# Kernel tuning notes

Measured on AMD Instinct MI355X. Metric: run time of the kernel, lower is better.

Reference implementation:

```python
import jax, jax.numpy as jnp
import numpy as np

N_NODES = 100000
N_EDGES = 1600000
IN_FEATS = 128
N_HIDDEN = 64
N_HEADS = 4
N_CLASSES = 16


def setup_inputs() -> dict:
    key = jax.random.key(0)
    ks = jax.random.split(key, 16)
    h = jax.random.normal(ks[0], (N_NODES, IN_FEATS), dtype=jnp.float32)
    src = jax.random.randint(ks[1], (N_EDGES,), 0, N_NODES, dtype=jnp.int32)
    dst = jax.random.randint(ks[2], (N_EDGES,), 0, N_NODES, dtype=jnp.int32)
    def xavier(k, shape, fan_in, fan_out):
        gain = jnp.sqrt(2.0)  # calculate_gain('relu')
        std = gain * jnp.sqrt(2.0 / (fan_in + fan_out))
        return (std * jax.random.normal(k, shape)).astype(jnp.float32)
    # layer 1: per-head W [H, in, out], A [H, 2*out]
    W1 = xavier(ks[3], (N_HEADS, IN_FEATS, N_HIDDEN), IN_FEATS, N_HIDDEN)
    b1 = jnp.zeros((N_HEADS, N_HIDDEN), jnp.float32)
    a1 = xavier(ks[4], (N_HEADS, 2 * N_HIDDEN), 2 * N_HIDDEN, 1)
    ab1 = jnp.zeros((N_HEADS,), jnp.float32)
    # layer 2: input is concat of heads = N_HEADS*N_HIDDEN, output n_classes, heads averaged
    d2 = N_HEADS * N_HIDDEN
    W2 = xavier(ks[5], (N_HEADS, d2, N_CLASSES), d2, N_CLASSES)
    b2 = jnp.zeros((N_HEADS, N_CLASSES), jnp.float32)
    a2 = xavier(ks[6], (N_HEADS, 2 * N_CLASSES), 2 * N_CLASSES, 1)
    ab2 = jnp.zeros((N_HEADS,), jnp.float32)
    fc_w = xavier(ks[7], (N_CLASSES, N_CLASSES), N_CLASSES, N_CLASSES)
    fc_b = jnp.zeros((N_CLASSES,), jnp.float32)
    return dict(h=h, src=src, dst=dst, W1=W1, b1=b1, a1=a1, ab1=ab1,
                W2=W2, b2=b2, a2=a2, ab2=ab2, fc_w=fc_w, fc_b=fc_b)


def gat_layer(h, src, dst, W, b, a, ab, n_nodes):
    # h: [N, F]; W: [H, F, O]; a: [H, 2O]
    O = W.shape[-1]
    Wh = jnp.einsum('nf,hfo->nho', h, W) + b          # [N, H, O]
    Wh_src = Wh[src]                                   # [E, H, O] (messages Wh_j)
    Wh_dst = Wh[dst]                                   # [E, H, O] (Wh_i)
    # e_ij = LeakyReLU(A([Wh_i, Wh_j]), 0.2)
    e = (jnp.einsum('eho,ho->eh', Wh_dst, a[:, :O])
         + jnp.einsum('eho,ho->eh', Wh_src, a[:, O:]) + ab)  # [E, H]
    e = jax.nn.leaky_relu(e, 0.2)
    # segment softmax over incoming edges of each dst node
    m = jax.ops.segment_max(e, dst, num_segments=n_nodes)     # [N, H] (-inf for empty)
    ex = jnp.exp(e - m[dst])
    denom = jax.ops.segment_sum(ex, dst, num_segments=n_nodes)
    alpha = ex / denom[dst]                                    # [E, H]
    # weighted neighbor aggregation (zero for zero-in-degree nodes, as DGL)
    out = jax.ops.segment_sum(alpha[:, :, None] * Wh_src, dst, num_segments=n_nodes)
    return out  # [N, H, O]


def reference(h, src, dst, W1, b1, a1, ab1, W2, b2, a2, ab2, fc_w, fc_b):
    n = h.shape[0]
    # layer 1 (heads concatenated) + ELU; dropout = identity (eval mode)
    h1 = gat_layer(h, src, dst, W1, b1, a1, ab1, n)            # [N, H, n_hidden]
    h1 = jax.nn.elu(h1.reshape(n, -1))                         # [N, H*n_hidden]
    # layer 2 (heads averaged) + softmax over features
    h2 = gat_layer(h1, src, dst, W2, b2, a2, ab2, n).mean(axis=1)  # [N, n_classes]
    h2 = jax.nn.softmax(h2, axis=1)
    # readout: mean over nodes, then fc
    hg = h2.mean(axis=0)                                        # [n_classes]
    return hg @ fc_w.T + fc_b
```

## Files before the change

kernel.cpp:

```cpp
#include <hip/hip_runtime.h>
#include <math.h>

#define N_NODES  100000
#define N_EDGES  1600000
#define IN_F     128
#define HID      64
#define HEADS    4
#define NCLS     16
#define D1       (HEADS*HID)
#define D2       (HEADS*NCLS)

#define SCAN_CHUNK 1024
#define SCAN_NB    ((N_NODES + SCAN_CHUNK - 1) / SCAN_CHUNK)
#define N_NODES_PAD (SCAN_NB * SCAN_CHUNK)
#define RB1 128

typedef __attribute__((ext_vector_type(8))) short bf16x8_t;
typedef __attribute__((ext_vector_type(4))) float f32x4_t;
typedef __attribute__((ext_vector_type(2))) float f32x2_t;

__device__ __forceinline__ unsigned bf16rne(float x) {
  unsigned u = __float_as_uint(x);
  return (u + 0x7fffu + ((u >> 16) & 1u)) >> 16;
}
__device__ __forceinline__ unsigned packbf2(float lo, float hi) {
  return bf16rne(lo) | (bf16rne(hi) << 16);
}
__device__ __forceinline__ float bflo(unsigned p) { return __uint_as_float(p << 16); }
__device__ __forceinline__ float bfhi(unsigned p) { return __uint_as_float(p & 0xffff0000u); }

__global__ __launch_bounds__(256)
void k_zero4(int4* __restrict__ p, int n4) {
  int i = blockIdx.x * blockDim.x + threadIdx.x;
  if (i < n4) p[i] = make_int4(0, 0, 0, 0);
}

__global__ __launch_bounds__(256)
void k_count(const int* __restrict__ dst, int* __restrict__ cursorPad,
             int* __restrict__ rank) {
  int i = blockIdx.x * blockDim.x + threadIdx.x;
  if (i < N_EDGES) {
    int d = dst[i];
    rank[i] = atomicAdd(&cursorPad[d << 4], 1);
  }
}

__global__ __launch_bounds__(256)
void k_compact(const int* __restrict__ cursorPad, int* __restrict__ counts) {
  int i = blockIdx.x * blockDim.x + threadIdx.x;
  if (i < N_NODES_PAD) counts[i] = (i < N_NODES) ? cursorPad[i << 4] : 0;
}

__global__ __launch_bounds__(256)
void k_scanA(const int* __restrict__ counts, int* __restrict__ btot) {
  __shared__ int red[256];
  int t = threadIdx.x;
  const int4* cp = (const int4*)(counts + blockIdx.x * SCAN_CHUNK);
  int4 v = cp[t];
  red[t] = v.x + v.y + v.z + v.w;
  __syncthreads();
  for (int s = 128; s; s >>= 1) {
    if (t < s) red[t] += red[t + s];
    __syncthreads();
  }
  if (t == 0) btot[blockIdx.x] = red[0];
}

__global__ __launch_bounds__(128)
void k_scanB(const int* __restrict__ btot, int* __restrict__ bbase,
             int* __restrict__ offs) {
  __shared__ int part[128];
  int t = threadIdx.x;
  part[t] = (t < SCAN_NB) ? btot[t] : 0;
  __syncthreads();
  for (int o = 1; o < 128; o <<= 1) {
    int v = (t >= o) ? part[t - o] : 0;
    __syncthreads();
    part[t] += v;
    __syncthreads();
  }
  if (t < SCAN_NB) bbase[t] = (t == 0) ? 0 : part[t - 1];
  if (t == 0) offs[N_NODES] = N_EDGES;
}

__global__ __launch_bounds__(256)
void k_scanC(const int* __restrict__ counts, const int* __restrict__ bbase,
             int* __restrict__ offs) {
  __shared__ int part[256];
  int t = threadIdx.x;
  int gbase = blockIdx.x * SCAN_CHUNK;
  const int4* cp = (const int4*)(counts + gbase);
  int4 v = cp[t];
  int tot = v.x + v.y + v.z + v.w;
  part[t] = tot;
  __syncthreads();
  for (int o = 1; o < 256; o <<= 1) {
    int q = (t >= o) ? part[t - o] : 0;
    __syncthreads();
    part[t] += q;
    __syncthreads();
  }
  int run = bbase[blockIdx.x] + part[t] - tot;
  int i0 = gbase + t * 4;
  int o0 = run;
  int o1 = o0 + v.x;
  int o2 = o1 + v.y;
  int o3 = o2 + v.z;
  if (i0 + 0 < N_NODES) offs[i0 + 0] = o0;
  if (i0 + 1 < N_NODES) offs[i0 + 1] = o1;
  if (i0 + 2 < N_NODES) offs[i0 + 2] = o2;
  if (i0 + 3 < N_NODES) offs[i0 + 3] = o3;
}

__global__ __launch_bounds__(256)
void k_scatter(const int* __restrict__ src, const int* __restrict__ dst,
               const int* __restrict__ rank, const int* __restrict__ offs,
               int* __restrict__ csrsrc) {
  int i = blockIdx.x * blockDim.x + threadIdx.x;
  if (i < N_EDGES) {
    csrsrc[offs[dst[i]] + rank[i]] = src[i];
  }
}

__global__ __launch_bounds__(256)
void k_prepw(const float* __restrict__ W1, const float* __restrict__ W2,
             unsigned* __restrict__ W1t32, unsigned* __restrict__ W2t32) {
  int t = threadIdx.x;
  if (blockIdx.x == 0) {
    int c = t;
    const float* wp = W1 + ((c >> 6) << 13) + (c & 63);
    unsigned* op = W1t32 + c * 64;
    for (int fp = 0; fp < 64; ++fp) {
      float lo = wp[(2 * fp) << 6];
      float hi = wp[(2 * fp + 1) << 6];
      op[fp] = packbf2(lo, hi);
    }
  } else {
    int c = t & 63, fq = t >> 6;
    const float* wp = W2 + ((c >> 4) << 12) + (c & 15);
    unsigned* op = W2t32 + c * 128 + fq * 32;
    for (int fp = 0; fp < 32; ++fp) {
      int f0 = fq * 64 + 2 * fp;
      op[fp] = packbf2(wp[f0 << 4], wp[(f0 + 1) << 4]);
    }
  }
}

__global__ __launch_bounds__(256)
void k_gemm1(const float* __restrict__ h, const unsigned short* __restrict__ W1t,
             const float* __restrict__ bias, const float* __restrict__ a1,
             unsigned char* __restrict__ Wh8,
             float* __restrict__ sD, float* __restrict__ sS) {
  __shared__ float aLds[512];
  int t = threadIdx.x;
  aLds[t] = a1[t];
  aLds[t + 256] = a1[t + 256];
  __syncthreads();

  int wv = t >> 6;
  int lane = t & 63;
  int m = lane & 15;
  int q8 = (lane >> 4) * 8;
  int node = blockIdx.x * 64 + wv * 16 + m;
  int nclamp = node < N_NODES ? node : N_NODES - 1;

  f32x4_t acc[16] = {};
  const float* hp0 = h + (size_t)nclamp * IN_F + q8;
  #pragma unroll
  for (int ks = 0; ks < 4; ++ks) {
    int kk = ks * 32;
    float4 f0 = *(const float4*)(hp0 + kk);
    float4 f1 = *(const float4*)(hp0 + kk + 4);
    bf16x8_t bf;
    bf[0] = (short)bf16rne(f0.x); bf[1] = (short)bf16rne(f0.y);
    bf[2] = (short)bf16rne(f0.z); bf[3] = (short)bf16rne(f0.w);
    bf[4] = (short)bf16rne(f1.x); bf[5] = (short)bf16rne(f1.y);
    bf[6] = (short)bf16rne(f1.z); bf[7] = (short)bf16rne(f1.w);
    #pragma unroll
    for (int ct = 0; ct < 16; ++ct) {
      bf16x8_t af = *(const bf16x8_t*)(W1t + (ct * 16 + m) * IN_F + kk + q8);
      acc[ct] = __builtin_amdgcn_mfma_f32_16x16x32_bf16(af, bf, acc[ct], 0, 0, 0);
    }
  }
  if (node < N_NODES) {
    unsigned char* op = Wh8 + (size_t)node * D1;
    int quad4 = (lane >> 4) * 4;
    float pd[4] = {}, ps[4] = {};
    #pragma unroll
    for (int ct = 0; ct < 16; ++ct) {
      int c0 = ct * 16 + quad4;
      float4 bb = *(const float4*)(bias + c0);
      float v0 = acc[ct][0] + bb.x, v1 = acc[ct][1] + bb.y;
      float v2 = acc[ct][2] + bb.z, v3 = acc[ct][3] + bb.w;
      int hh = ct >> 2;
      const float* aD = &aLds[hh * 128 + (c0 & 63)];
      pd[hh] += v0 * aD[0] + v1 * aD[1] + v2 * aD[2] + v3 * aD[3];
      ps[hh] += v0 * aD[64] + v1 * aD[65] + v2 * aD[66] + v3 * aD[67];
      int pk = __builtin_amdgcn_cvt_pk_fp8_f32(v0, v1, 0, false);
      pk = __builtin_amdgcn_cvt_pk_fp8_f32(v2, v3, pk, true);
      *(unsigned*)(op + c0) = (unsigned)pk;
    }
    #pragma unroll
    for (int hh = 0; hh < 4; ++hh) {
      pd[hh] += __shfl_xor(pd[hh], 16); pd[hh] += __shfl_xor(pd[hh], 32);
      ps[hh] += __shfl_xor(ps[hh], 16); ps[hh] += __shfl_xor(ps[hh], 32);
    }
    if (lane < 16) {
      ((float4*)sD)[node] = make_float4(pd[0], pd[1], pd[2], pd[3]);
      ((float4*)sS)[node] = make_float4(ps[0], ps[1], ps[2], ps[3]);
    }
  }
}

__global__ __launch_bounds__(256)
void k_gemm2(const unsigned short* __restrict__ h1b, const unsigned short* __restrict__ W2t,
             const float* __restrict__ bias, const float* __restrict__ a2,
             unsigned short* __restrict__ Whb2,
             float* __restrict__ sD, float* __restrict__ sS) {
  __shared__ float aLds[128];
  int t = threadIdx.x;
  if (t < 128) aLds[t] = a2[t];
  __syncthreads();

  int wv = t >> 6;
  int lane = t & 63;
  int m = lane & 15;
  int q8 = (lane >> 4) * 8;
  int node = blockIdx.x * 64 + wv * 16 + m;
  int nclamp = node < N_NODES ? node : N_NODES - 1;

  f32x4_t acc[4] = {};
  const unsigned short* hp0 = h1b + (size_t)nclamp * D1 + q8;
  #pragma unroll
  for (int ks = 0; ks < 8; ++ks) {
    int kk = ks * 32;
    bf16x8_t bf = *(const bf16x8_t*)(hp0 + kk);
    #pragma unroll
    for (int ct = 0; ct < 4; ++ct) {
      bf16x8_t af = *(const bf16x8_t*)(W2t + (ct * 16 + m) * D1 + kk + q8);
      acc[ct] = __builtin_amdgcn_mfma_f32_16x16x32_bf16(af, bf, acc[ct], 0, 0, 0);
    }
  }
  if (node < N_NODES) {
    unsigned short* op = Whb2 + (size_t)node * D2;
    int quad4 = (lane >> 4) * 4;
    float pd[4] = {}, ps[4] = {};
    #pragma unroll
    for (int ct = 0; ct < 4; ++ct) {
      int c0 = ct * 16 + quad4;
      float4 bb = *(const float4*)(bias + c0);
      float v0 = acc[ct][0] + bb.x, v1 = acc[ct][1] + bb.y;
      float v2 = acc[ct][2] + bb.z, v3 = acc[ct][3] + bb.w;
      const float* aD = &aLds[ct * 32 + (c0 & 15)];
      pd[ct] += v0 * aD[0] + v1 * aD[1] + v2 * aD[2] + v3 * aD[3];
      ps[ct] += v0 * aD[16] + v1 * aD[17] + v2 * aD[18] + v3 * aD[19];
      uint2 o;
      o.x = packbf2(v0, v1);
      o.y = packbf2(v2, v3);
      *(uint2*)(op + c0) = o;
    }
    #pragma unroll
    for (int hh = 0; hh < 4; ++hh) {
      pd[hh] += __shfl_xor(pd[hh], 16); pd[hh] += __shfl_xor(pd[hh], 32);
      ps[hh] += __shfl_xor(ps[hh], 16); ps[hh] += __shfl_xor(ps[hh], 32);
    }
    if (lane < 16) {
      ((float4*)sD)[node] = make_float4(pd[0], pd[1], pd[2], pd[3]);
      ((float4*)sS)[node] = make_float4(ps[0], ps[1], ps[2], ps[3]);
    }
  }
}

__device__ __forceinline__ float lrelu(float x) { return x > 0.f ? x : 0.2f * x; }
__device__ __forceinline__ float elu(float x)   { return x > 0.f ? x : expm1f(x); }

__global__ __launch_bounds__(256)
void k_agg1(const int* __restrict__ offs, const int* __restrict__ csrsrc,
            const float* __restrict__ sD, const float* __restrict__ sS,
            const float* __restrict__ ab,
            const unsigned char* __restrict__ Wh8, unsigned short* __restrict__ h1out) {
  __shared__ float exbuf[4][64 * 4];
  __shared__ int   offbuf[4][64];
  int wv = threadIdx.x >> 6;
  int wid = blockIdx.x * 4 + wv;
  int lane = threadIdx.x & 63;
  int g = lane >> 5;
  int l = lane & 31;
  int hh = l >> 3;
  f32x2_t acc[4] = {};
  float z0 = 0.f, z1 = 0.f, z2 = 0.f, z3 = 0.f;
  int beg = offs[wid], end = offs[wid + 1];
  bool nonempty = end > beg;
  const char* rowbase = (const char*)Wh8 + (l << 3);
  if (nonempty) {
    float4 dv = ((const float4*)sD)[wid];
    float db0 = dv.x + ab[0], db1 = dv.y + ab[1];
    float db2 = dv.z + ab[2], db3 = dv.w + ab[3];
    const float* eb = exbuf[wv];
    const int* ob = offbuf[wv];
    for (int cbeg = beg; cbeg < end; cbeg += 64) {
      int j = cbeg + lane;
      int cnt = end - cbeg; if (cnt > 64) cnt = 64;
      int sid = 0;
      float e0 = 0.f, e1 = 0.f, e2 = 0.f, e3 = 0.f;
      if (j < end) {
        sid = csrsrc[j];
        float4 sv = ((const float4*)sS)[sid];
        e0 = __expf(lrelu(db0 + sv.x));
        e1 = __expf(lrelu(db1 + sv.y));
        e2 = __expf(lrelu(db2 + sv.z));
        e3 = __expf(lrelu(db3 + sv.w));
        z0 += e0; z1 += e1; z2 += e2; z3 += e3;
      }
      offbuf[wv][lane] = sid << 8;
      *(float4*)&exbuf[wv][lane * 4] = make_float4(e0, e1, e2, e3);
      int npairs = (cnt + 1) >> 1;
      for (int u = 0; u < npairs; ++u) {
        int i0 = 2 * u + g;
        float w = eb[i0 * 4 + hh];
        int off = ob[i0];
        uint2 p = *(const uint2*)(rowbase + off);
        f32x2_t w2; w2[0] = w; w2[1] = w;
        acc[0] = __builtin_elementwise_fma(__builtin_amdgcn_cvt_pk_f32_fp8(p.x, false), w2, acc[0]);
        acc[1] = __builtin_elementwise_fma(__builtin_amdgcn_cvt_pk_f32_fp8(p.x, true),  w2, acc[1]);
        acc[2] = __builtin_elementwise_fma(__builtin_amdgcn_cvt_pk_f32_fp8(p.y, false), w2, acc[2]);
        acc[3] = __builtin_elementwise_fma(__builtin_amdgcn_cvt_pk_f32_fp8(p.y, true),  w2, acc[3]);
      }
    }
    #pragma unroll
    for (int o = 32; o; o >>= 1) {
      z0 += __shfl_xor(z0, o);
      z1 += __shfl_xor(z1, o);
      z2 += __shfl_xor(z2, o);
      z3 += __shfl_xor(z3, o);
    }
  }
  #pragma unroll
  for (int i = 0; i < 4; ++i) {
    acc[i][0] += __shfl_xor(acc[i][0], 32);
    acc[i][1] += __shfl_xor(acc[i][1], 32);
  }
  float z = (hh == 0) ? z0 : (hh == 1) ? z1 : (hh == 2) ? z2 : z3;
  if (!nonempty) z = 1.f;
  float inv = 1.f / z;
  if (g == 0) {
    float e0 = elu(acc[0][0] * inv), e1 = elu(acc[0][1] * inv);
    float e2 = elu(acc[1][0] * inv), e3 = elu(acc[1][1] * inv);
    float e4 = elu(acc[2][0] * inv), e5 = elu(acc[2][1] * inv);
    float e6 = elu(acc[3][0] * inv), e7 = elu(acc[3][1] * inv);
    uint4 o;
    o.x = packbf2(e0, e1);
    o.y = packbf2(e2, e3);
    o.z = packbf2(e4, e5);
    o.w = packbf2(e6, e7);
    *(uint4*)(h1out + (size_t)wid * D1 + l * 8) = o;
  }
}

__global__ __launch_bounds__(256)
void k_agg2(const int* __restrict__ offs, const int* __restrict__ csrsrc,
            const float* __restrict__ sD, const float* __restrict__ sS,
            const float* __restrict__ ab,
            const unsigned short* __restrict__ Whb2, float* __restrict__ partials) {
  __shared__ float exbuf[4][64 * 4];
  __shared__ int   offbuf[4][64];
  __shared__ float red[4][16];
  int wv = threadIdx.x >> 6;
  int wid = blockIdx.x * 4 + wv;
  int lane = threadIdx.x & 63;
  int g = lane >> 4;
  int l = lane & 15;
  int hh = l >> 2;
  float acc[4] = {};
  float z0 = 0.f, z1 = 0.f, z2 = 0.f, z3 = 0.f;
  int beg = offs[wid], end = offs[wid + 1];
  bool nonempty = end > beg;
  if (nonempty) {
    float4 dv = ((const float4*)sD)[wid];
    float db0 = dv.x + ab[0], db1 = dv.y + ab[1];
    float db2 = dv.z + ab[2], db3 = dv.w + ab[3];
    const float* eb = exbuf[wv];
    const int* ob = offbuf[wv];
    for (int cbeg = beg; cbeg < end; cbeg += 64) {
      int j = cbeg + lane;
      int cnt = end - cbeg; if (cnt > 64) cnt = 64;
      if (j < end) {
        int sid = csrsrc[j];
        float4 sv = ((const float4*)sS)[sid];
        float e0 = __expf(lrelu(db0 + sv.x));
        float e1 = __expf(lrelu(db1 + sv.y));
        float e2 = __expf(lrelu(db2 + sv.z));
        float e3 = __expf(lrelu(db3 + sv.w));
        z0 += e0; z1 += e1; z2 += e2; z3 += e3;
        offbuf[wv][lane] = sid << 7;
        *(float4*)&exbuf[wv][lane * 4] = make_float4(e0, e1, e2, e3);
      }
      int iters = (cnt + 3) >> 2;
      for (int it = 0; it < iters; ++it) {
        int qq = 4 * it + g;
        int idx = qq < cnt ? qq : cnt - 1;
        float w = eb[idx * 4 + hh];
        if (qq >= cnt) w = 0.f;
        int off = ob[idx];
        uint2 p = *(const uint2*)((const char*)Whb2 + off + (l << 3));
        acc[0] = fmaf(w, __uint_as_float(p.x << 16), acc[0]);
        acc[1] = fmaf(w, __uint_as_float(p.x), acc[1]);
        acc[2] = fmaf(w, __uint_as_float(p.y << 16), acc[2]);
        acc[3] = fmaf(w, __uint_as_float(p.y), acc[3]);
      }
    }
    #pragma unroll
    for (int s = 32; s; s >>= 1) {
      z0 += __shfl_xor(z0, s);
      z1 += __shfl_xor(z1, s);
      z2 += __shfl_xor(z2, s);
      z3 += __shfl_xor(z3, s);
    }
  }
  #pragma unroll
  for (int i = 0; i < 4; ++i) {
    acc[i] += __shfl_xor(acc[i], 16);
    acc[i] += __shfl_xor(acc[i], 32);
  }
  float z = (hh == 0) ? z0 : (hh == 1) ? z1 : (hh == 2) ? z2 : z3;
  if (!nonempty) z = 1.f;
  float inv = 1.f / z;
  float val[4];
  #pragma unroll
  for (int i = 0; i < 4; ++i) val[i] = acc[i] * inv;
  #pragma unroll
  for (int i = 0; i < 4; ++i) {
    val[i] += __shfl_xor(val[i], 4);
    val[i] += __shfl_xor(val[i], 8);
    val[i] *= 0.25f;
  }
  float mx = fmaxf(fmaxf(val[0], val[1]), fmaxf(val[2], val[3]));
  mx = fmaxf(mx, __shfl_xor(mx, 1));
  mx = fmaxf(mx, __shfl_xor(mx, 2));
  float e[4];
  float ssum = 0.f;
  #pragma unroll
  for (int i = 0; i < 4; ++i) { e[i] = __expf(val[i] - mx); ssum += e[i]; }
  ssum += __shfl_xor(ssum, 1);
  ssum += __shfl_xor(ssum, 2);
  float rinv = 1.f / ssum;
  if (g == 0 && l < 4) {
    #pragma unroll
    for (int i = 0; i < 4; ++i) red[wv][l * 4 + i] = e[i] * rinv;
  }
  __syncthreads();
  if (threadIdx.x < 16) {
    partials[(size_t)blockIdx.x * 16 + threadIdx.x] =
        red[0][threadIdx.x] + red[1][threadIdx.x] +
        red[2][threadIdx.x] + red[3][threadIdx.x];
  }
}

__global__ __launch_bounds__(256)
void k_reduce1(const float* __restrict__ partials, int nrows,
               float* __restrict__ out) {
  __shared__ float red[16][17];
  int t = threadIdx.x;
  int c = t & 15, rl = t >> 4;
  int per = (nrows + RB1 - 1) / RB1;
  int rbeg = blockIdx.x * per;
  int rend = rbeg + per; if (rend > nrows) rend = nrows;
  float s = 0.f;
  for (int r = rbeg + rl; r < rend; r += 16) s += partials[(size_t)r * 16 + c];
  red[rl][c] = s;
  __syncthreads();
  for (int st = 8; st; st >>= 1) {
    if (rl < st) red[rl][c] += red[rl + st][c];
    __syncthreads();
  }
  if (t < 16) out[(size_t)blockIdx.x * 16 + t] = red[0][t];
}

__global__ __launch_bounds__(256)
void k_final(const float* __restrict__ partials,
             const float* __restrict__ fcw, const float* __restrict__ fcb,
             float* __restrict__ out) {
  __shared__ float red[16][17];
  __shared__ float hg[16];
  int t = threadIdx.x;
  int c = t & 15, rl = t >> 4;
  float s = 0.f;
  for (int r = rl; r < RB1; r += 16) s += partials[(size_t)r * 16 + c];
  red[rl][c] = s;
  __syncthreads();
  for (int st = 8; st; st >>= 1) {
    if (rl < st) red[rl][c] += red[rl + st][c];
    __syncthreads();
  }
  if (t < 16) hg[t] = red[0][t] * (1.0f / N_NODES);
  __syncthreads();
  if (t < 16) {
    float acc = fcb[t];
    #pragma unroll
    for (int k = 0; k < 16; ++k) acc += hg[k] * fcw[t * 16 + k];
    out[t] = acc;
  }
}

extern "C" void kernel_launch(void* const* d_in, const int* in_sizes, int n_in,
                              void* d_out, int out_size, void* d_ws, size_t ws_size,
                              hipStream_t stream) {
  const float* h   = (const float*)d_in[0];
  const int*   src = (const int*)  d_in[1];
  const int*   dst = (const int*)  d_in[2];
  const float* W1  = (const float*)d_in[3];
  const float* b1  = (const float*)d_in[4];
  const float* a1  = (const float*)d_in[5];
  const float* ab1 = (const float*)d_in[6];
  const float* W2  = (const float*)d_in[7];
  const float* b2  = (const float*)d_in[8];
  const float* a2  = (const float*)d_in[9];
  const float* ab2 = (const float*)d_in[10];
  const float* fcw = (const float*)d_in[11];
  const float* fcb = (const float*)d_in[12];
  float* out = (float*)d_out;

  char* ws = (char*)d_ws;
  size_t off = 0;
  auto alloc = [&](size_t bytes) -> char* {
    char* p = ws + off;
    off += (bytes + 255) & ~(size_t)255;
    return p;
  };
  unsigned char*  Wh8  = (unsigned char*)alloc((size_t)N_NODES * D1);
  unsigned short* h1b  = (unsigned short*)alloc((size_t)N_NODES * D1 * 2);
  unsigned short* Whb2 = (unsigned short*)alloc((size_t)N_NODES * D2 * 2);
  unsigned short* W1t  = (unsigned short*)alloc((size_t)D1 * IN_F * 2);
  unsigned short* W2t  = (unsigned short*)alloc((size_t)D2 * D1 * 2);
  float* sD1 = (float*)alloc((size_t)N_NODES * 4 * 4);
  float* sS1 = (float*)alloc((size_t)N_NODES * 4 * 4);
  float* sD2 = (float*)alloc((size_t)N_NODES * 4 * 4);
  float* sS2 = (float*)alloc((size_t)N_NODES * 4 * 4);
  int* cursorPad = (int*)alloc((size_t)N_NODES * 16 * 4);
  int* rank   = (int*)alloc((size_t)N_EDGES * 4);
  int* counts = (int*)alloc((size_t)N_NODES_PAD * 4);
  int* offs   = (int*)alloc((size_t)(N_NODES + 1) * 4);
  int* csrsrc = (int*)alloc((size_t)N_EDGES * 4);
  int* btot   = (int*)alloc((size_t)SCAN_NB * 4);
  int* bbase  = (int*)alloc((size_t)SCAN_NB * 4);
  const int nblk_node = (N_NODES + 3) / 4;
  float* partials  = (float*)alloc((size_t)nblk_node * 16 * 4);
  float* partials2 = (float*)alloc((size_t)RB1 * 16 * 4);

  k_prepw<<<2, 256, 0, stream>>>(W1, W2, (unsigned*)W1t, (unsigned*)W2t);

  const int n4 = N_NODES * 4;
  k_zero4<<<(n4 + 255) / 256, 256, 0, stream>>>((int4*)cursorPad, n4);
  k_count<<<(N_EDGES + 255) / 256, 256, 0, stream>>>(dst, cursorPad, rank);
  k_compact<<<(N_NODES_PAD + 255) / 256, 256, 0, stream>>>(cursorPad, counts);
  k_scanA<<<SCAN_NB, 256, 0, stream>>>(counts, btot);
  k_scanB<<<1, 128, 0, stream>>>(btot, bbase, offs);
  k_scanC<<<SCAN_NB, 256, 0, stream>>>(counts, bbase, offs);
  k_scatter<<<(N_EDGES + 255) / 256, 256, 0, stream>>>(src, dst, rank, offs, csrsrc);

  const int gemmBlocks = (N_NODES + 63) / 64;

  k_gemm1<<<gemmBlocks, 256, 0, stream>>>(h, W1t, b1, a1, Wh8, sD1, sS1);
  k_agg1<<<nblk_node, 256, 0, stream>>>(offs, csrsrc, sD1, sS1, ab1, Wh8, h1b);

  k_gemm2<<<gemmBlocks, 256, 0, stream>>>(h1b, W2t, b2, a2, Whb2, sD2, sS2);
  k_agg2<<<nblk_node, 256, 0, stream>>>(offs, csrsrc, sD2, sS2, ab2, Whb2, partials);

  k_reduce1<<<RB1, 256, 0, stream>>>(partials, nblk_node, partials2);
  k_final<<<1, 256, 0, stream>>>(partials2, fcw, fcb, out);
}
```

Before: 480.6 us.

## Store layer-2 features in FP8 and drop padded atomic counter buffer

Layer-2 projected features are now written as FP8 instead of bf16, which halves the bytes gathered per edge in the second aggregation. The aggregation uses packed FP8-to-float conversion and paired FMAs, and its inner loop no longer clamps the index because zero weights are written to shared memory for lanes past the edge count. The degree count now does its atomics directly into the compact counts array, which removes the 16-way padded cursor buffer and the compaction kernel. The costs are lower precision on layer-2 messages and more atomic contention on adjacent counters.

```diff
diff --git a/kernel.cpp b/kernel.cpp
--- a/kernel.cpp
+++ b/kernel.cpp
@@ -36,19 +36,12 @@
 }
 
 __global__ __launch_bounds__(256)
-void k_count(const int* __restrict__ dst, int* __restrict__ cursorPad,
+void k_count(const int* __restrict__ dst, int* __restrict__ counts,
              int* __restrict__ rank) {
   int i = blockIdx.x * blockDim.x + threadIdx.x;
   if (i < N_EDGES) {
-    int d = dst[i];
-    rank[i] = atomicAdd(&cursorPad[d << 4], 1);
-  }
-}
-
-__global__ __launch_bounds__(256)
-void k_compact(const int* __restrict__ cursorPad, int* __restrict__ counts) {
-  int i = blockIdx.x * blockDim.x + threadIdx.x;
-  if (i < N_NODES_PAD) counts[i] = (i < N_NODES) ? cursorPad[i << 4] : 0;
+    rank[i] = atomicAdd(&counts[dst[i]], 1);
+  }
 }
 
 __global__ __launch_bounds__(256)
@@ -215,7 +208,7 @@
 __global__ __launch_bounds__(256)
 void k_gemm2(const unsigned short* __restrict__ h1b, const unsigned short* __restrict__ W2t,
              const float* __restrict__ bias, const float* __restrict__ a2,
-             unsigned short* __restrict__ Whb2,
+             unsigned char* __restrict__ Wh2_8,
              float* __restrict__ sD, float* __restrict__ sS) {
   __shared__ float aLds[128];
   int t = threadIdx.x;
@@ -242,7 +235,7 @@
     }
   }
   if (node < N_NODES) {
-    unsigned short* op = Whb2 + (size_t)node * D2;
+    unsigned char* op = Wh2_8 + (size_t)node * D2;
     int quad4 = (lane >> 4) * 4;
     float pd[4] = {}, ps[4] = {};
     #pragma unroll
@@ -254,10 +247,9 @@
       const float* aD = &aLds[ct * 32 + (c0 & 15)];
       pd[ct] += v0 * aD[0] + v1 * aD[1] + v2 * aD[2] + v3 * aD[3];
       ps[ct] += v0 * aD[16] + v1 * aD[17] + v2 * aD[18] + v3 * aD[19];
-      uint2 o;
-      o.x = packbf2(v0, v1);
-      o.y = packbf2(v2, v3);
-      *(uint2*)(op + c0) = o;
+      int pk = __builtin_amdgcn_cvt_pk_fp8_f32(v0, v1, 0, false);
+      pk = __builtin_amdgcn_cvt_pk_fp8_f32(v2, v3, pk, true);
+      *(unsigned*)(op + c0) = (unsigned)pk;
     }
     #pragma unroll
     for (int hh = 0; hh < 4; ++hh) {
@@ -361,7 +353,7 @@
 void k_agg2(const int* __restrict__ offs, const int* __restrict__ csrsrc,
             const float* __restrict__ sD, const float* __restrict__ sS,
             const float* __restrict__ ab,
-            const unsigned short* __restrict__ Whb2, float* __restrict__ partials) {
+            const unsigned char* __restrict__ Wh2_8, float* __restrict__ partials) {
   __shared__ float exbuf[4][64 * 4];
   __shared__ int   offbuf[4][64];
   __shared__ float red[4][16];
@@ -371,10 +363,11 @@
   int g = lane >> 4;
   int l = lane & 15;
   int hh = l >> 2;
-  float acc[4] = {};
+  f32x2_t acc[2] = {};
   float z0 = 0.f, z1 = 0.f, z2 = 0.f, z3 = 0.f;
   int beg = offs[wid], end = offs[wid + 1];
   bool nonempty = end > beg;
+  const char* rowbase = (const char*)Wh2_8 + (l << 2);
   if (nonempty) {
     float4 dv = ((const float4*)sD)[wid];
     float db0 = dv.x + ab[0], db1 = dv.y + ab[1];
@@ -384,29 +377,28 @@
     for (int cbeg = beg; cbeg < end; cbeg += 64) {
       int j = cbeg + lane;
       int cnt = end - cbeg; if (cnt > 64) cnt = 64;
+      int sid = 0;
+      float e0 = 0.f, e1 = 0.f, e2 = 0.f, e3 = 0.f;
       if (j < end) {
-        int sid = csrsrc[j];
+        sid = csrsrc[j];
         float4 sv = ((const float4*)sS)[sid];
-        float e0 = __expf(lrelu(db0 + sv.x));
-        float e1 = __expf(lrelu(db1 + sv.y));
-        float e2 = __expf(lrelu(db2 + sv.z));
-        float e3 = __expf(lrelu(db3 + sv.w));
+        e0 = __expf(lrelu(db0 + sv.x));
+        e1 = __expf(lrelu(db1 + sv.y));
+        e2 = __expf(lrelu(db2 + sv.z));
+        e3 = __expf(lrelu(db3 + sv.w));
         z0 += e0; z1 += e1; z2 += e2; z3 += e3;
-        offbuf[wv][lane] = sid << 7;
-        *(float4*)&exbuf[wv][lane * 4] = make_float4(e0, e1, e2, e3);
       }
-      int iters = (cnt + 3) >> 2;
-      for (int it = 0; it < iters; ++it) {
-        int qq = 4 * it + g;
-        int idx = qq < cnt ? qq : cnt - 1;
-        float w = eb[idx * 4 + hh];
-        if (qq >= cnt) w = 0.f;
-        int off = ob[idx];
-        uint2 p = *(const uint2*)((const char*)Whb2 + off + (l << 3));
-        acc[0] = fmaf(w, __uint_as_float(p.x << 16), acc[0]);
-        acc[1] = fmaf(w, __uint_as_float(p.x), acc[1]);
-        acc[2] = fmaf(w, __uint_as_float(p.y << 16), acc[2]);
-        acc[3] = fmaf(w, __uint_as_float(p.y), acc[3]);
+      offbuf[wv][lane] = sid << 6;
+      *(float4*)&exbuf[wv][lane * 4] = make_float4(e0, e1, e2, e3);
+      int nq = (cnt + 3) >> 2;
+      for (int u = 0; u < nq; ++u) {
+        int i0 = 4 * u + g;
+        float w = eb[i0 * 4 + hh];
+        int off = ob[i0];
+        unsigned p = *(const unsigned*)(rowbase + off);
+        f32x2_t w2; w2[0] = w; w2[1] = w;
+        acc[0] = __builtin_elementwise_fma(__builtin_amdgcn_cvt_pk_f32_fp8(p, false), w2, acc[0]);
+        acc[1] = __builtin_elementwise_fma(__builtin_amdgcn_cvt_pk_f32_fp8(p, true),  w2, acc[1]);
       }
     }
     #pragma unroll
@@ -418,16 +410,18 @@
     }
   }
   #pragma unroll
-  for (int i = 0; i < 4; ++i) {
-    acc[i] += __shfl_xor(acc[i], 16);
-    acc[i] += __shfl_xor(acc[i], 32);
+  for (int i = 0; i < 2; ++i) {
+    acc[i][0] += __shfl_xor(acc[i][0], 16);
+    acc[i][1] += __shfl_xor(acc[i][1], 16);
+    acc[i][0] += __shfl_xor(acc[i][0], 32);
+    acc[i][1] += __shfl_xor(acc[i][1], 32);
   }
   float z = (hh == 0) ? z0 : (hh == 1) ? z1 : (hh == 2) ? z2 : z3;
   if (!nonempty) z = 1.f;
   float inv = 1.f / z;
   float val[4];
-  #pragma unroll
-  for (int i = 0; i < 4; ++i) val[i] = acc[i] * inv;
+  val[0] = acc[0][0] * inv; val[1] = acc[0][1] * inv;
+  val[2] = acc[1][0] * inv; val[3] = acc[1][1] * inv;
   #pragma unroll
   for (int i = 0; i < 4; ++i) {
     val[i] += __shfl_xor(val[i], 4);
@@ -527,16 +521,15 @@
     off += (bytes + 255) & ~(size_t)255;
     return p;
   };
-  unsigned char*  Wh8  = (unsigned char*)alloc((size_t)N_NODES * D1);
-  unsigned short* h1b  = (unsigned short*)alloc((size_t)N_NODES * D1 * 2);
-  unsigned short* Whb2 = (unsigned short*)alloc((size_t)N_NODES * D2 * 2);
-  unsigned short* W1t  = (unsigned short*)alloc((size_t)D1 * IN_F * 2);
-  unsigned short* W2t  = (unsigned short*)alloc((size_t)D2 * D1 * 2);
+  unsigned char*  Wh8   = (unsigned char*)alloc((size_t)N_NODES * D1);
+  unsigned short* h1b   = (unsigned short*)alloc((size_t)N_NODES * D1 * 2);
+  unsigned char*  Wh2_8 = (unsigned char*)alloc((size_t)N_NODES * D2);
+  unsigned short* W1t   = (unsigned short*)alloc((size_t)D1 * IN_F * 2);
+  unsigned short* W2t   = (unsigned short*)alloc((size_t)D2 * D1 * 2);
   float* sD1 = (float*)alloc((size_t)N_NODES * 4 * 4);
   float* sS1 = (float*)alloc((size_t)N_NODES * 4 * 4);
   float* sD2 = (float*)alloc((size_t)N_NODES * 4 * 4);
   float* sS2 = (float*)alloc((size_t)N_NODES * 4 * 4);
-  int* cursorPad = (int*)alloc((size_t)N_NODES * 16 * 4);
   int* rank   = (int*)alloc((size_t)N_EDGES * 4);
   int* counts = (int*)alloc((size_t)N_NODES_PAD * 4);
   int* offs   = (int*)alloc((size_t)(N_NODES + 1) * 4);
@@ -549,10 +542,9 @@
 
   k_prepw<<<2, 256, 0, stream>>>(W1, W2, (unsigned*)W1t, (unsigned*)W2t);
 
-  const int n4 = N_NODES * 4;
-  k_zero4<<<(n4 + 255) / 256, 256, 0, stream>>>((int4*)cursorPad, n4);
-  k_count<<<(N_EDGES + 255) / 256, 256, 0, stream>>>(dst, cursorPad, rank);
-  k_compact<<<(N_NODES_PAD + 255) / 256, 256, 0, stream>>>(cursorPad, counts);
+  const int n4 = N_NODES_PAD / 4;
+  k_zero4<<<(n4 + 255) / 256, 256, 0, stream>>>((int4*)counts, n4);
+  k_count<<<(N_EDGES + 255) / 256, 256, 0, stream>>>(dst, counts, rank);
   k_scanA<<<SCAN_NB, 256, 0, stream>>>(counts, btot);
   k_scanB<<<1, 128, 0, stream>>>(btot, bbase, offs);
   k_scanC<<<SCAN_NB, 256, 0, stream>>>(counts, bbase, offs);
@@ -563,8 +555,8 @@
   k_gemm1<<<gemmBlocks, 256, 0, stream>>>(h, W1t, b1, a1, Wh8, sD1, sS1);
   k_agg1<<<nblk_node, 256, 0, stream>>>(offs, csrsrc, sD1, sS1, ab1, Wh8, h1b);
 
-  k_gemm2<<<gemmBlocks, 256, 0, stream>>>(h1b, W2t, b2, a2, Whb2, sD2, sS2);
-  k_agg2<<<nblk_node, 256, 0, stream>>>(offs, csrsrc, sD2, sS2, ab2, Whb2, partials);
+  k_gemm2<<<gemmBlocks, 256, 0, stream>>>(h1b, W2t, b2, a2, Wh2_8, sD2, sS2);
+  k_agg2<<<nblk_node, 256, 0, stream>>>(offs, csrsrc, sD2, sS2, ab2, Wh2_8, partials);
 
   k_reduce1<<<RB1, 256, 0, stream>>>(partials, nblk_node, partials2);
   k_final<<<1, 256, 0, stream>>>(partials2, fcw, fcb, out);
```

Result: slower. 498.3 us (+3.7%).
